# Kernel tuning notes

Measured on AMD Instinct MI355X. Metric: run time of the kernel, lower is better.

The kernel has to match this reference:

```python
import jax, jax.numpy as jnp
import numpy as np


def setup_inputs() -> dict:
    key = jax.random.key(0)
    kq, kk, kv = jax.random.split(key, 3)
    B, H, S, D = 2, 16, 2048, 128
    return {
        "q": jax.random.normal(kq, (B, H, S, D), dtype=jnp.float32),
        "k": jax.random.normal(kk, (B, H, S, D), dtype=jnp.float32),
        "v": jax.random.normal(kv, (B, H, S, D), dtype=jnp.float32),
    }


def reference(q, k, v):
    # scaled dot-product attention with causal mask (dropout in eval mode -> identity)
    d_k = k.shape[-1]
    scale = 1.0 / jnp.sqrt(jnp.asarray(d_k, dtype=q.dtype))
    # [B,H,Sq,Skv]
    attn = jnp.einsum("bhqd,bhkd->bhqk", q, k) * scale
    Sq = q.shape[-2]
    causal = jnp.triu(jnp.ones((Sq, Sq), dtype=bool), k=1)  # True above diagonal -> masked
    attn = jnp.where(causal, -jnp.inf, attn)
    attn = jax.nn.softmax(attn, axis=-1)
    return jnp.einsum("bhqk,bhkd->bhqd", attn, v)
```

## Files before the change

### kernel.cpp

```cpp
#include <hip/hip_runtime.h>

#define SQ 2048
#define DH 128
#define KVB 64
#define BHN 32
#define ELEMS ((size_t)BHN * SQ * DH)

typedef __bf16 bf16x8 __attribute__((ext_vector_type(8)));
typedef float f32x16 __attribute__((ext_vector_type(16)));

__device__ __forceinline__ f32x16 mfma32(bf16x8 a, bf16x8 b, f32x16 c){
  return __builtin_amdgcn_mfma_f32_32x32x16_bf16(a, b, c, 0, 0, 0);
}

#define EXP2 __builtin_amdgcn_exp2f
#define GLD16(g, l) __builtin_amdgcn_global_load_lds( \
    (const __attribute__((address_space(1))) void*)(g), \
    (__attribute__((address_space(3))) void*)(l), 16, 0, 0)
#define VMCNT0 asm volatile("s_waitcnt vmcnt(0)" ::: "memory")
#define VMCNT4 asm volatile("s_waitcnt vmcnt(4)" ::: "memory")
#define VMCNT8 asm volatile("s_waitcnt vmcnt(8)" ::: "memory")
#define BARRIER asm volatile("s_barrier" ::: "memory")

__device__ __forceinline__ unsigned short f2bf(float f){
  unsigned u = __builtin_bit_cast(unsigned, f);
  u += 0x7fffu + ((u >> 16) & 1u);
  return (unsigned short)(u >> 16);
}
__device__ __forceinline__ unsigned packbf(float a, float b){
  return (unsigned)f2bf(a) | ((unsigned)f2bf(b) << 16);
}

__device__ __forceinline__ void swap32(unsigned a, unsigned b, bool h, unsigned &x, unsigned &y){
  unsigned sb = __shfl_xor(b, 32);
  unsigned sa = __shfl_xor(a, 32);
  x = h ? sb : a;
  y = h ? b : sa;
}

__device__ __forceinline__ bf16x8 mkfrag(unsigned w0, unsigned w1, unsigned w2, unsigned w3){
  uint4 t; t.x = w0; t.y = w1; t.z = w2; t.w = w3;
  return __builtin_bit_cast(bf16x8, t);
}

__global__ __launch_bounds__(256, 4)
void convk(const float* __restrict__ K, unsigned short* __restrict__ Kb){
  const size_t g = (size_t)blockIdx.x * 256 + threadIdx.x;
  #pragma unroll
  for (int i = 0; i < 4; ++i){
    size_t e = (g + (size_t)i * 262144) * 8;
    float4 a = *(const float4*)(K + e);
    float4 b = *(const float4*)(K + e + 4);
    uint4 o;
    o.x = packbf(a.x, a.y); o.y = packbf(a.z, a.w);
    o.z = packbf(b.x, b.y); o.w = packbf(b.z, b.w);
    *(uint4*)(Kb + e) = o;
  }
}

__global__ __launch_bounds__(256, 4)
void convvt(const float* __restrict__ V, unsigned short* __restrict__ Vt){
  __shared__ unsigned short T[64][65];
  const int bidx = blockIdx.x;
  const int dt = bidx & 1;
  const int kt = (bidx >> 1) & 31;
  const int bh = bidx >> 6;
  const float* src = V + (size_t)bh*SQ*DH + (size_t)kt*64*DH + dt*64;
  unsigned short* dst = Vt + (size_t)bh*DH*SQ + (size_t)dt*64*SQ + kt*64;
  const int t = threadIdx.x;
  const int c4 = (t & 15) * 4;
  const int r0 = t >> 4;
  #pragma unroll
  for (int i = 0; i < 4; ++i){
    int r = r0 + i*16;
    float4 f = *(const float4*)(src + (size_t)r*DH + c4);
    T[r][c4+0] = f2bf(f.x); T[r][c4+1] = f2bf(f.y);
    T[r][c4+2] = f2bf(f.z); T[r][c4+3] = f2bf(f.w);
  }
  __syncthreads();
  #pragma unroll
  for (int i = 0; i < 4; ++i){
    int d = r0 + i*16;
    ushort4 w;
    w.x = T[c4+0][d]; w.y = T[c4+1][d]; w.z = T[c4+2][d]; w.w = T[c4+3][d];
    *(ushort4*)(dst + (size_t)d*SQ + c4) = w;
  }
}

__global__ __launch_bounds__(512, 2)
void attn_fwd_gl(const float* __restrict__ Q,
                 const unsigned short* __restrict__ Kbg,
                 const unsigned short* __restrict__ Vtg,
                 float* __restrict__ O)
{
  __shared__ __align__(16) unsigned char smem[131072];
  float* SF = (float*)smem;

  const int tid  = threadIdx.x;
  const int lane = tid & 63;
  const int wid  = tid >> 6;
  const int rg   = wid & 3;
  const int par  = wid >> 2;
  const int col  = lane & 31;
  const int hi   = lane >> 5;

  const int b   = blockIdx.x;
  const int xcd = b & 7;
  const int seq = b >> 3;
  const int bh4 = seq & 3;
  const int j   = seq >> 2;
  const int bh  = xcd + 8*bh4;

  const size_t base = (size_t)bh * SQ * DH;
  const float* Qg = Q + base;
  const unsigned short* Kb = Kbg + base;
  const unsigned short* Vt = Vtg + base;
  float* Og = O + base;

  const float SC = 0.08838834764831845f * 1.4426950408889634f;

  const unsigned short* ksrc[2];
  const unsigned short* vsrc[2];
  int kdst[2], vdst[2];
  #pragma unroll
  for (int i = 0; i < 2; ++i){
    int c = i*512 + tid;
    int r = c >> 4, dc = c & 15;
    ksrc[i] = Kb + (size_t)r*DH + ((dc ^ (r & 7)) * 8);
    kdst[i] = c * 16;
    int d = c >> 3, f = c & 7;
    vsrc[i] = Vt + (size_t)d*SQ + ((f ^ ((d >> 1) & 7)) * 8);
    vdst[i] = 16384 + c * 16;
  }

  auto LOADT = [&](int kvb, int bsel){
    const int bboff = bsel * 32768;
    #pragma unroll
    for (int i = 0; i < 2; ++i){
      GLD16(ksrc[i] + (size_t)kvb * DH, &smem[bboff + kdst[i]]);
      GLD16(vsrc[i] + kvb,              &smem[bboff + vdst[i]]);
    }
  };

  #pragma unroll 1
  for (int ph = 0; ph < 2; ++ph){
    const int qt = ph ? j : (15 - j);
    const int nt = 2*qt + 2;
    const int Q0 = qt*128 + rg*32;
    const int qg = Q0 + col;

    bf16x8 qf[8];
    #pragma unroll
    for (int dc = 0; dc < 8; ++dc){
      const float* src = Qg + (size_t)qg*DH + dc*16 + hi*8;
      float4 f0 = *(const float4*)(src);
      float4 f1 = *(const float4*)(src + 4);
      uint4 tq;
      tq.x = packbf(f0.x*SC, f0.y*SC); tq.y = packbf(f0.z*SC, f0.w*SC);
      tq.z = packbf(f1.x*SC, f1.y*SC); tq.w = packbf(f1.z*SC, f1.w*SC);
      qf[dc] = __builtin_bit_cast(bf16x8, tq);
    }

    f32x16 o0 = {}, o1 = {}, o2 = {}, o3 = {};
    float m = -1e30f, lsum = 0.f;

    LOADT(0, 0);
    if (nt > 1) LOADT(KVB, 1);
    if (nt > 2) LOADT(2*KVB, 2);
    if (nt > 2){ VMCNT8; } else { VMCNT4; }
    BARRIER;

    #pragma unroll 1
    for (int t = 0; t < nt; ++t){
      const int kvb = t * KVB;
      const int bboff = (t & 3) * 32768;
      const int myk = kvb + par*32;

      if (t + 3 < nt) LOADT(kvb + 3*KVB, (t + 3) & 3);

      if (myk <= Q0 + 31){
        f32x16 s0 = {};
        const int krow = par*32 + col;
        #pragma unroll
        for (int dc = 0; dc < 8; ++dc){
          uint4 rk = *(const uint4*)&smem[bboff + krow*256 + ((dc*32 + hi*16) ^ ((krow & 7) << 4))];
          s0 = mfma32(__builtin_bit_cast(bf16x8, rk), qf[dc], s0);
        }

        if (myk + 31 > Q0){
          #pragma unroll
          for (int r = 0; r < 16; ++r){
            int kl = (r & 3) + 8*(r >> 2) + 4*hi;
            if (myk + kl > qg) s0[r] = -1e30f;
          }
        }

        float tmax = -1e30f;
        #pragma unroll
        for (int r = 0; r < 16; ++r) tmax = fmaxf(tmax, s0[r]);
        tmax = fmaxf(tmax, __shfl_xor(tmax, 32));
        if (!__all(tmax <= m + 8.0f)){
          float mnew  = fmaxf(m, tmax);
          float alpha = EXP2(m - mnew);
          m = mnew;
          lsum *= alpha;
          o0 *= alpha; o1 *= alpha; o2 *= alpha; o3 *= alpha;
        }

        float ps = 0.f;
        #pragma unroll
        for (int r = 0; r < 16; ++r){ float e = EXP2(s0[r] - m); s0[r] = e; ps += e; }
        lsum += ps;

        unsigned ua0 = packbf(s0[0],  s0[1]),  ua1 = packbf(s0[2],  s0[3]);
        unsigned ua2 = packbf(s0[4],  s0[5]),  ua3 = packbf(s0[6],  s0[7]);
        unsigned ua4 = packbf(s0[8],  s0[9]),  ua5 = packbf(s0[10], s0[11]);
        unsigned ua6 = packbf(s0[12], s0[13]), ua7 = packbf(s0[14], s0[15]);
        bool h = (bool)hi;
        unsigned w0, w1, w2, w3;
        bf16x8 pf[2];
        swap32(ua0, ua2, h, w0, w2); swap32(ua1, ua3, h, w1, w3); pf[0] = mkfrag(w0,w1,w2,w3);
        swap32(ua4, ua6, h, w0, w2); swap32(ua5, ua7, h, w1, w3); pf[1] = mkfrag(w0,w1,w2,w3);

        #pragma unroll
        for (int cc = 0; cc < 2; ++cc){
          #pragma unroll
          for (int db = 0; db < 4; ++db){
            int rowd = db*32 + col;
            uint4 rv = *(const uint4*)&smem[bboff + 16384 + rowd*128 + ((par*64 + cc*32 + hi*16) ^ (((rowd >> 1) & 7) << 4))];
            f32x16& oo = (db==0)?o0:(db==1)?o1:(db==2)?o2:o3;
            oo = mfma32(__builtin_bit_cast(bf16x8, rv), pf[cc], oo);
          }
        }
      }

      if (t + 1 < nt){
        const int rem = nt - 2 - t;
        if (rem >= 2){ VMCNT8; } else if (rem == 1){ VMCNT4; } else { VMCNT0; }
      }
      BARRIER;
    }

    lsum += __shfl_xor(lsum, 32);

    float a0 = 1.f, a1 = 0.f, inv = 0.f;
    #pragma unroll 1
    for (int round = 0; round < 2; ++round){
      const f32x16& pa = round ? o2 : o0;
      const f32x16& pb = round ? o3 : o1;
      if (par == 1){
        #pragma unroll
        for (int i2 = 0; i2 < 16; ++i2){
          SF[rg*2048 + i2*64 + lane]      = pa[i2];
          SF[rg*2048 + (16+i2)*64 + lane] = pb[i2];
        }
        if (round == 0){
          SF[8192 + rg*64 + lane] = m;
          SF[8448 + rg*64 + lane] = lsum;
        }
      }
      __syncthreads();
      if (par == 0){
        if (round == 0){
          float m1 = SF[8192 + rg*64 + lane];
          float l1 = SF[8448 + rg*64 + lane];
          float ms = fmaxf(m, m1);
          a0 = EXP2(m - ms);
          a1 = EXP2(m1 - ms);
          float ls = lsum*a0 + l1*a1;
          inv = 1.0f / ls;
        }
        #pragma unroll
        for (int dbi = 0; dbi < 2; ++dbi){
          const f32x16& oo = round ? (dbi ? o3 : o2) : (dbi ? o1 : o0);
          const int db = round*2 + dbi;
          #pragma unroll
          for (int rg2 = 0; rg2 < 4; ++rg2){
            float4 w;
            w.x = (oo[rg2*4+0]*a0 + SF[rg*2048 + (dbi*16 + rg2*4+0)*64 + lane]*a1) * inv;
            w.y = (oo[rg2*4+1]*a0 + SF[rg*2048 + (dbi*16 + rg2*4+1)*64 + lane]*a1) * inv;
            w.z = (oo[rg2*4+2]*a0 + SF[rg*2048 + (dbi*16 + rg2*4+2)*64 + lane]*a1) * inv;
            w.w = (oo[rg2*4+3]*a0 + SF[rg*2048 + (dbi*16 + rg2*4+3)*64 + lane]*a1) * inv;
            *(float4*)(Og + (size_t)qg*DH + db*32 + rg2*8 + hi*4) = w;
          }
        }
      }
      __syncthreads();
    }
  }
}

__global__ __launch_bounds__(512, 2)
void attn_fwd_fb(const float* __restrict__ Q,
                 const float* __restrict__ Kf,
                 const float* __restrict__ Vf,
                 float* __restrict__ O)
{
  __shared__ __align__(16) unsigned char smem[65536];
  float* SF = (float*)smem;
  const int tid  = threadIdx.x;
  const int lane = tid & 63;
  const int wid  = tid >> 6;
  const int rg   = wid & 3;
  const int par  = wid >> 2;
  const int col  = lane & 31;
  const int hi   = lane >> 5;
  const int i4   = lane & 3;
  const int d0   = (lane >> 2)*8;
  const int b   = blockIdx.x;
  const int xcd = b & 7;
  const int seq = b >> 3;
  const int bh4 = seq & 3;
  const int j   = seq >> 2;
  const int bh  = xcd + 8*bh4;
  const size_t base = (size_t)bh * SQ * DH;
  const float* Qg = Q + base;
  const float* Kg = Kf + base;
  const float* Vg = Vf + base;
  float* Og = O + base;
  const float SC = 0.08838834764831845f * 1.4426950408889634f;
  float4 kr[4], vr[4];
  auto LOADT = [&](int kvb){
    #pragma unroll
    for (int i2 = 0; i2 < 2; ++i2){
      int c = i2*512 + tid, r = c >> 4, dc = c & 15;
      const float* src = Kg + (size_t)(kvb + r)*DH + dc*8;
      kr[2*i2]   = *(const float4*)(src);
      kr[2*i2+1] = *(const float4*)(src + 4);
    }
    #pragma unroll
    for (int it = 0; it < 2; ++it){
      int row = wid*8 + it*4 + i4;
      const float* src = Vg + (size_t)(kvb + row)*DH + d0;
      vr[2*it]   = *(const float4*)(src);
      vr[2*it+1] = *(const float4*)(src + 4);
    }
  };
  auto STORET = [&](int bsel){
    const int bboff = bsel * 32768;
    #pragma unroll
    for (int i2 = 0; i2 < 2; ++i2){
      int c = i2*512 + tid, r = c >> 4, dc = c & 15;
      uint4 kv;
      kv.x = packbf(kr[2*i2].x,   kr[2*i2].y);
      kv.y = packbf(kr[2*i2].z,   kr[2*i2].w);
      kv.z = packbf(kr[2*i2+1].x, kr[2*i2+1].y);
      kv.w = packbf(kr[2*i2+1].z, kr[2*i2+1].w);
      *(uint4*)&smem[bboff + r*256 + ((dc*16) ^ ((r & 7) << 4))] = kv;
    }
    #pragma unroll
    for (int it = 0; it < 2; ++it){
      int r0 = wid*8 + it*4;
      unsigned M0 = packbf(vr[2*it].x,   vr[2*it].y);
      unsigned M1 = packbf(vr[2*it].z,   vr[2*it].w);
      unsigned M2 = packbf(vr[2*it+1].x, vr[2*it+1].y);
      unsigned M3 = packbf(vr[2*it+1].z, vr[2*it+1].w);
      unsigned t0=__shfl_xor(M1,1), t1=__shfl_xor(M0,1), t2=__shfl_xor(M3,1), t3=__shfl_xor(M2,1);
      bool ob1 = i4 & 1;
      unsigned N0 = ob1 ? t0 : M0;
      unsigned N1 = ob1 ? M1 : t1;
      unsigned N2 = ob1 ? t2 : M2;
      unsigned N3 = ob1 ? M3 : t3;
      unsigned u0s=__shfl_xor(N2,2), u1s=__shfl_xor(N3,2), u2s=__shfl_xor(N0,2), u3s=__shfl_xor(N1,2);
      bool ob2 = i4 & 2;
      unsigned F0 = ob2 ? u0s : N0;
      unsigned F1 = ob2 ? u1s : N1;
      unsigned F2 = ob2 ? N2 : u2s;
      unsigned F3 = ob2 ? N3 : u3s;
      int d = d0 + 2*i4;
      unsigned lo0 = (F0 & 0xffffu) | (F1 << 16);
      unsigned lo1 = (F2 & 0xffffu) | (F3 << 16);
      unsigned hi0 = (F0 >> 16) | (F1 & 0xffff0000u);
      unsigned hi1 = (F2 >> 16) | (F3 & 0xffff0000u);
      int cb = r0*2;
      int sA = ((d >> 1) & 7) << 4;
      *(uint2*)&smem[bboff + 16384 + d*128     + (cb ^ sA)] = make_uint2(lo0, lo1);
      *(uint2*)&smem[bboff + 16384 + (d+1)*128 + (cb ^ sA)] = make_uint2(hi0, hi1);
    }
  };
  #pragma unroll 1
  for (int ph = 0; ph < 2; ++ph){
    const int qt = ph ? j : (15 - j);
    const int nt = 2*qt + 2;
    const int Q0 = qt*128 + rg*32;
    const int qg = Q0 + col;
    bf16x8 qf[8];
    #pragma unroll
    for (int dc = 0; dc < 8; ++dc){
      const float* src = Qg + (size_t)qg*DH + dc*16 + hi*8;
      float4 f0 = *(const float4*)(src);
      float4 f1 = *(const float4*)(src + 4);
      uint4 tq;
      tq.x = packbf(f0.x*SC, f0.y*SC); tq.y = packbf(f0.z*SC, f0.w*SC);
      tq.z = packbf(f1.x*SC, f1.y*SC); tq.w = packbf(f1.z*SC, f1.w*SC);
      qf[dc] = __builtin_bit_cast(bf16x8, tq);
    }
    f32x16 o0 = {}, o1 = {}, o2 = {}, o3 = {};
    float m = -1e30f, lsum = 0.f;
    LOADT(0);
    STORET(0);
    __syncthreads();
    #pragma unroll 1
    for (int t = 0; t < nt; ++t){
      const int kvb = t * KVB;
      const int bboff = (t & 1) * 32768;
      const int myk = kvb + par*32;
      if (t + 1 < nt) LOADT(kvb + KVB);
      if (myk <= Q0 + 31){
        f32x16 s0 = {};
        const int krow = par*32 + col;
        #pragma unroll
        for (int dc = 0; dc < 8; ++dc){
          uint4 rk = *(const uint4*)&smem[bboff + krow*256 + ((dc*32 + hi*16) ^ ((krow & 7) << 4))];
          s0 = mfma32(__builtin_bit_cast(bf16x8, rk), qf[dc], s0);
        }
        if (myk + 31 > Q0){
          #pragma unroll
          for (int r = 0; r < 16; ++r){
            int kl = (r & 3) + 8*(r >> 2) + 4*hi;
            if (myk + kl > qg) s0[r] = -1e30f;
          }
        }
        float tmax = -1e30f;
        #pragma unroll
        for (int r = 0; r < 16; ++r) tmax = fmaxf(tmax, s0[r]);
        tmax = fmaxf(tmax, __shfl_xor(tmax, 32));
        if (!__all(tmax <= m + 8.0f)){
          float mnew  = fmaxf(m, tmax);
          float alpha = EXP2(m - mnew);
          m = mnew;
          lsum *= alpha;
          o0 *= alpha; o1 *= alpha; o2 *= alpha; o3 *= alpha;
        }
        float ps = 0.f;
        #pragma unroll
        for (int r = 0; r < 16; ++r){ float e = EXP2(s0[r] - m); s0[r] = e; ps += e; }
        lsum += ps;
        unsigned ua0 = packbf(s0[0],  s0[1]),  ua1 = packbf(s0[2],  s0[3]);
        unsigned ua2 = packbf(s0[4],  s0[5]),  ua3 = packbf(s0[6],  s0[7]);
        unsigned ua4 = packbf(s0[8],  s0[9]),  ua5 = packbf(s0[10], s0[11]);
        unsigned ua6 = packbf(s0[12], s0[13]), ua7 = packbf(s0[14], s0[15]);
        bool h = (bool)hi;
        unsigned w0, w1, w2, w3;
        bf16x8 pf[2];
        swap32(ua0, ua2, h, w0, w2); swap32(ua1, ua3, h, w1, w3); pf[0] = mkfrag(w0,w1,w2,w3);
        swap32(ua4, ua6, h, w0, w2); swap32(ua5, ua7, h, w1, w3); pf[1] = mkfrag(w0,w1,w2,w3);
        #pragma unroll
        for (int cc = 0; cc < 2; ++cc){
          #pragma unroll
          for (int db = 0; db < 4; ++db){
            int rowd = db*32 + col;
            uint4 rv = *(const uint4*)&smem[bboff + 16384 + rowd*128 + ((par*64 + cc*32 + hi*16) ^ (((rowd >> 1) & 7) << 4))];
            f32x16& oo = (db==0)?o0:(db==1)?o1:(db==2)?o2:o3;
            oo = mfma32(__builtin_bit_cast(bf16x8, rv), pf[cc], oo);
          }
        }
      }
      if (t + 1 < nt) STORET((t + 1) & 1);
      __syncthreads();
    }
    lsum += __shfl_xor(lsum, 32);
    float a0 = 1.f, a1 = 0.f, inv = 0.f;
    #pragma unroll 1
    for (int round = 0; round < 2; ++round){
      const f32x16& pa = round ? o2 : o0;
      const f32x16& pb = round ? o3 : o1;
      if (par == 1){
        #pragma unroll
        for (int i2 = 0; i2 < 16; ++i2){
          SF[rg*2048 + i2*64 + lane]      = pa[i2];
          SF[rg*2048 + (16+i2)*64 + lane] = pb[i2];
        }
        if (round == 0){
          SF[8192 + rg*64 + lane] = m;
          SF[8448 + rg*64 + lane] = lsum;
        }
      }
      __syncthreads();
      if (par == 0){
        if (round == 0){
          float m1 = SF[8192 + rg*64 + lane];
          float l1 = SF[8448 + rg*64 + lane];
          float ms = fmaxf(m, m1);
          a0 = EXP2(m - ms);
          a1 = EXP2(m1 - ms);
          float ls = lsum*a0 + l1*a1;
          inv = 1.0f / ls;
        }
        #pragma unroll
        for (int dbi = 0; dbi < 2; ++dbi){
          const f32x16& oo = round ? (dbi ? o3 : o2) : (dbi ? o1 : o0);
          const int db = round*2 + dbi;
          #pragma unroll
          for (int rg2 = 0; rg2 < 4; ++rg2){
            float4 w;
            w.x = (oo[rg2*4+0]*a0 + SF[rg*2048 + (dbi*16 + rg2*4+0)*64 + lane]*a1) * inv;
            w.y = (oo[rg2*4+1]*a0 + SF[rg*2048 + (dbi*16 + rg2*4+1)*64 + lane]*a1) * inv;
            w.z = (oo[rg2*4+2]*a0 + SF[rg*2048 + (dbi*16 + rg2*4+2)*64 + lane]*a1) * inv;
            w.w = (oo[rg2*4+3]*a0 + SF[rg*2048 + (dbi*16 + rg2*4+3)*64 + lane]*a1) * inv;
            *(float4*)(Og + (size_t)qg*DH + db*32 + rg2*8 + hi*4) = w;
          }
        }
      }
      __syncthreads();
    }
  }
}

extern "C" void kernel_launch(void* const* d_in, const int* in_sizes, int n_in,
                              void* d_out, int out_size, void* d_ws, size_t ws_size,
                              hipStream_t stream) {
  const float* q = (const float*)d_in[0];
  const float* k = (const float*)d_in[1];
  const float* v = (const float*)d_in[2];
  float* out = (float*)d_out;

  const size_t need = 2 * ELEMS * sizeof(unsigned short);
  if (ws_size >= need){
    unsigned short* kb = (unsigned short*)d_ws;
    unsigned short* vt = kb + ELEMS;
    convk<<<1024, 256, 0, stream>>>(k, kb);
    convvt<<<2048, 256, 0, stream>>>(v, vt);
    attn_fwd_gl<<<256, 512, 0, stream>>>(q, kb, vt, out);
  } else {
    attn_fwd_fb<<<256, 512, 0, stream>>>(q, k, v, out);
  }
}
```

Before: 92.00 us.

## Software-pipeline PV of previous tile with QK of current tile

Restructures the attention loop so that each iteration issues the P·V MFMAs for the previous KV tile alongside the Q·K MFMAs for the current tile. The goal is to hide the softmax and exp latency behind matrix work, with s_setprio raising wave priority around the MFMA block. The P fragments and the previous buffer offset now live across iterations, and a final P·V drain runs after the loop. Prefetch depth drops from three tiles ahead to two, with waitcnts adjusted, which trades some load-latency hiding for a ring slot kept live for the delayed P·V read.

```diff
diff --git a/kernel.cpp b/kernel.cpp
--- a/kernel.cpp
+++ b/kernel.cpp
@@ -19,7 +19,6 @@
     (__attribute__((address_space(3))) void*)(l), 16, 0, 0)
 #define VMCNT0 asm volatile("s_waitcnt vmcnt(0)" ::: "memory")
 #define VMCNT4 asm volatile("s_waitcnt vmcnt(4)" ::: "memory")
-#define VMCNT8 asm volatile("s_waitcnt vmcnt(8)" ::: "memory")
 #define BARRIER asm volatile("s_barrier" ::: "memory")
 
 __device__ __forceinline__ unsigned short f2bf(float f){
@@ -163,11 +162,13 @@
 
     f32x16 o0 = {}, o1 = {}, o2 = {}, o3 = {};
     float m = -1e30f, lsum = 0.f;
+    bf16x8 pf0 = {}, pf1 = {};
+    bool pvalid = false;
+    int  prevbb = 0;
 
     LOADT(0, 0);
-    if (nt > 1) LOADT(KVB, 1);
-    if (nt > 2) LOADT(2*KVB, 2);
-    if (nt > 2){ VMCNT8; } else { VMCNT4; }
+    LOADT(KVB, 1);
+    VMCNT4;
     BARRIER;
 
     #pragma unroll 1
@@ -175,18 +176,36 @@
       const int kvb = t * KVB;
       const int bboff = (t & 3) * 32768;
       const int myk = kvb + par*32;
-
-      if (t + 3 < nt) LOADT(kvb + 3*KVB, (t + 3) & 3);
-
-      if (myk <= Q0 + 31){
-        f32x16 s0 = {};
+      const bool qvalid = (myk <= Q0 + 31);
+
+      if (t + 2 < nt) LOADT(kvb + 2*KVB, (t + 2) & 3);
+
+      f32x16 s0 = {};
+      __builtin_amdgcn_s_setprio(1);
+      if (pvalid){
+        #pragma unroll
+        for (int cc = 0; cc < 2; ++cc){
+          bf16x8 pf = cc ? pf1 : pf0;
+          #pragma unroll
+          for (int db = 0; db < 4; ++db){
+            int rowd = db*32 + col;
+            uint4 rv = *(const uint4*)&smem[prevbb + 16384 + rowd*128 + ((par*64 + cc*32 + hi*16) ^ (((rowd >> 1) & 7) << 4))];
+            f32x16& oo = (db==0)?o0:(db==1)?o1:(db==2)?o2:o3;
+            oo = mfma32(__builtin_bit_cast(bf16x8, rv), pf, oo);
+          }
+        }
+      }
+      if (qvalid){
         const int krow = par*32 + col;
         #pragma unroll
         for (int dc = 0; dc < 8; ++dc){
           uint4 rk = *(const uint4*)&smem[bboff + krow*256 + ((dc*32 + hi*16) ^ ((krow & 7) << 4))];
           s0 = mfma32(__builtin_bit_cast(bf16x8, rk), qf[dc], s0);
         }
-
+      }
+      __builtin_amdgcn_s_setprio(0);
+
+      if (qvalid){
         if (myk + 31 > Q0){
           #pragma unroll
           for (int r = 0; r < 16; ++r){
@@ -218,28 +237,34 @@
         unsigned ua6 = packbf(s0[12], s0[13]), ua7 = packbf(s0[14], s0[15]);
         bool h = (bool)hi;
         unsigned w0, w1, w2, w3;
-        bf16x8 pf[2];
-        swap32(ua0, ua2, h, w0, w2); swap32(ua1, ua3, h, w1, w3); pf[0] = mkfrag(w0,w1,w2,w3);
-        swap32(ua4, ua6, h, w0, w2); swap32(ua5, ua7, h, w1, w3); pf[1] = mkfrag(w0,w1,w2,w3);
-
-        #pragma unroll
-        for (int cc = 0; cc < 2; ++cc){
-          #pragma unroll
-          for (int db = 0; db < 4; ++db){
-            int rowd = db*32 + col;
-            uint4 rv = *(const uint4*)&smem[bboff + 16384 + rowd*128 + ((par*64 + cc*32 + hi*16) ^ (((rowd >> 1) & 7) << 4))];
-            f32x16& oo = (db==0)?o0:(db==1)?o1:(db==2)?o2:o3;
-            oo = mfma32(__builtin_bit_cast(bf16x8, rv), pf[cc], oo);
-          }
-        }
-      }
+        swap32(ua0, ua2, h, w0, w2); swap32(ua1, ua3, h, w1, w3); pf0 = mkfrag(w0,w1,w2,w3);
+        swap32(ua4, ua6, h, w0, w2); swap32(ua5, ua7, h, w1, w3); pf1 = mkfrag(w0,w1,w2,w3);
+      }
+      pvalid = qvalid;
+      prevbb = bboff;
 
       if (t + 1 < nt){
-        const int rem = nt - 2 - t;
-        if (rem >= 2){ VMCNT8; } else if (rem == 1){ VMCNT4; } else { VMCNT0; }
+        if (t + 2 < nt){ VMCNT4; } else { VMCNT0; }
       }
       BARRIER;
     }
+
+    __builtin_amdgcn_s_setprio(1);
+    if (pvalid){
+      #pragma unroll
+      for (int cc = 0; cc < 2; ++cc){
+        bf16x8 pf = cc ? pf1 : pf0;
+        #pragma unroll
+        for (int db = 0; db < 4; ++db){
+          int rowd = db*32 + col;
+          uint4 rv = *(const uint4*)&smem[prevbb + 16384 + rowd*128 + ((par*64 + cc*32 + hi*16) ^ (((rowd >> 1) & 7) << 4))];
+          f32x16& oo = (db==0)?o0:(db==1)?o1:(db==2)?o2:o3;
+          oo = mfma32(__builtin_bit_cast(bf16x8, rv), pf, oo);
+        }
+      }
+    }
+    __builtin_amdgcn_s_setprio(0);
+    __syncthreads();
 
     lsum += __shfl_xor(lsum, 32);
 
```

New measurement: 94.00 us. 1.02x slower.

## Merge K/V conversion launches and use permlane32 swap for cross-half exchanges

Applied to the files above, without the earlier changes.

Combines the K bf16 conversion and V transpose-conversion kernels into one launch with a block-index split, removing a kernel launch and its tail gap. In the attention inner loop, the ds_bpermute-based __shfl_xor(…,32) exchanges for the row max, P fragment repacking and final lsum are replaced by the v_permlane32_swap instruction. The max reduction is also rewritten as a tree to shorten the dependency chain. The permlane swap semantics must match the old select-based swap; they do if the instruction swaps the upper half of the first operand with the lower half of the second.

```diff
diff --git a/kernel.cpp b/kernel.cpp
--- a/kernel.cpp
+++ b/kernel.cpp
@@ -8,6 +8,7 @@
 
 typedef __bf16 bf16x8 __attribute__((ext_vector_type(8)));
 typedef float f32x16 __attribute__((ext_vector_type(16)));
+typedef unsigned uint2v __attribute__((ext_vector_type(2)));
 
 __device__ __forceinline__ f32x16 mfma32(bf16x8 a, bf16x8 b, f32x16 c){
   return __builtin_amdgcn_mfma_f32_32x32x16_bf16(a, b, c, 0, 0, 0);
@@ -31,6 +32,29 @@
   return (unsigned)f2bf(a) | ((unsigned)f2bf(b) << 16);
 }
 
+#if __has_builtin(__builtin_amdgcn_permlane32_swap)
+__device__ __forceinline__ void swap32p(unsigned a, unsigned b, unsigned &x, unsigned &y){
+  uint2v r = __builtin_amdgcn_permlane32_swap(a, b, false, false);
+  x = r[0]; y = r[1];
+}
+#else
+__device__ __forceinline__ void swap32p(unsigned a, unsigned b, unsigned &x, unsigned &y){
+  x = a; y = b;
+  asm volatile("" : "+v"(x), "+v"(y));
+  asm("v_permlane32_swap_b32 %0, %1" : "+v"(x), "+v"(y));
+}
+#endif
+__device__ __forceinline__ float halfmax(float t){
+  unsigned u = __builtin_bit_cast(unsigned, t), x, y;
+  swap32p(u, u, x, y);
+  return fmaxf(__builtin_bit_cast(float, x), __builtin_bit_cast(float, y));
+}
+__device__ __forceinline__ float halfadd(float t){
+  unsigned u = __builtin_bit_cast(unsigned, t), x, y;
+  swap32p(u, u, x, y);
+  return __builtin_bit_cast(float, x) + __builtin_bit_cast(float, y);
+}
+
 __device__ __forceinline__ void swap32(unsigned a, unsigned b, bool h, unsigned &x, unsigned &y){
   unsigned sb = __shfl_xor(b, 32);
   unsigned sa = __shfl_xor(a, 32);
@@ -44,46 +68,46 @@
 }
 
 __global__ __launch_bounds__(256, 4)
-void convk(const float* __restrict__ K, unsigned short* __restrict__ Kb){
-  const size_t g = (size_t)blockIdx.x * 256 + threadIdx.x;
-  #pragma unroll
-  for (int i = 0; i < 4; ++i){
-    size_t e = (g + (size_t)i * 262144) * 8;
-    float4 a = *(const float4*)(K + e);
-    float4 b = *(const float4*)(K + e + 4);
-    uint4 o;
-    o.x = packbf(a.x, a.y); o.y = packbf(a.z, a.w);
-    o.z = packbf(b.x, b.y); o.w = packbf(b.z, b.w);
-    *(uint4*)(Kb + e) = o;
-  }
-}
-
-__global__ __launch_bounds__(256, 4)
-void convvt(const float* __restrict__ V, unsigned short* __restrict__ Vt){
-  __shared__ unsigned short T[64][65];
-  const int bidx = blockIdx.x;
-  const int dt = bidx & 1;
-  const int kt = (bidx >> 1) & 31;
-  const int bh = bidx >> 6;
-  const float* src = V + (size_t)bh*SQ*DH + (size_t)kt*64*DH + dt*64;
-  unsigned short* dst = Vt + (size_t)bh*DH*SQ + (size_t)dt*64*SQ + kt*64;
-  const int t = threadIdx.x;
-  const int c4 = (t & 15) * 4;
-  const int r0 = t >> 4;
-  #pragma unroll
-  for (int i = 0; i < 4; ++i){
-    int r = r0 + i*16;
-    float4 f = *(const float4*)(src + (size_t)r*DH + c4);
-    T[r][c4+0] = f2bf(f.x); T[r][c4+1] = f2bf(f.y);
-    T[r][c4+2] = f2bf(f.z); T[r][c4+3] = f2bf(f.w);
-  }
-  __syncthreads();
-  #pragma unroll
-  for (int i = 0; i < 4; ++i){
-    int d = r0 + i*16;
-    ushort4 w;
-    w.x = T[c4+0][d]; w.y = T[c4+1][d]; w.z = T[c4+2][d]; w.w = T[c4+3][d];
-    *(ushort4*)(dst + (size_t)d*SQ + c4) = w;
+void convkvt(const float* __restrict__ K, const float* __restrict__ V,
+             unsigned short* __restrict__ Kb, unsigned short* __restrict__ Vt){
+  if (blockIdx.x < 1024){
+    const size_t g = (size_t)blockIdx.x * 256 + threadIdx.x;
+    #pragma unroll
+    for (int i = 0; i < 4; ++i){
+      size_t e = (g + (size_t)i * 262144) * 8;
+      float4 a = *(const float4*)(K + e);
+      float4 b = *(const float4*)(K + e + 4);
+      uint4 o;
+      o.x = packbf(a.x, a.y); o.y = packbf(a.z, a.w);
+      o.z = packbf(b.x, b.y); o.w = packbf(b.z, b.w);
+      *(uint4*)(Kb + e) = o;
+    }
+  } else {
+    __shared__ unsigned short T[64][65];
+    const int bidx = blockIdx.x - 1024;
+    const int dt = bidx & 1;
+    const int kt = (bidx >> 1) & 31;
+    const int bh = bidx >> 6;
+    const float* src = V + (size_t)bh*SQ*DH + (size_t)kt*64*DH + dt*64;
+    unsigned short* dst = Vt + (size_t)bh*DH*SQ + (size_t)dt*64*SQ + kt*64;
+    const int t = threadIdx.x;
+    const int c4 = (t & 15) * 4;
+    const int r0 = t >> 4;
+    #pragma unroll
+    for (int i = 0; i < 4; ++i){
+      int r = r0 + i*16;
+      float4 f = *(const float4*)(src + (size_t)r*DH + c4);
+      T[r][c4+0] = f2bf(f.x); T[r][c4+1] = f2bf(f.y);
+      T[r][c4+2] = f2bf(f.z); T[r][c4+3] = f2bf(f.w);
+    }
+    __syncthreads();
+    #pragma unroll
+    for (int i = 0; i < 4; ++i){
+      int d = r0 + i*16;
+      ushort4 w;
+      w.x = T[c4+0][d]; w.y = T[c4+1][d]; w.z = T[c4+2][d]; w.w = T[c4+3][d];
+      *(ushort4*)(dst + (size_t)d*SQ + c4) = w;
+    }
   }
 }
 
@@ -195,10 +219,13 @@
           }
         }
 
-        float tmax = -1e30f;
-        #pragma unroll
-        for (int r = 0; r < 16; ++r) tmax = fmaxf(tmax, s0[r]);
-        tmax = fmaxf(tmax, __shfl_xor(tmax, 32));
+        float p0 = fmaxf(s0[0],  s0[1]),  p1 = fmaxf(s0[2],  s0[3]);
+        float p2 = fmaxf(s0[4],  s0[5]),  p3 = fmaxf(s0[6],  s0[7]);
+        float p4 = fmaxf(s0[8],  s0[9]),  p5 = fmaxf(s0[10], s0[11]);
+        float p6 = fmaxf(s0[12], s0[13]), p7 = fmaxf(s0[14], s0[15]);
+        float q0v = fmaxf(p0, p1), q1v = fmaxf(p2, p3);
+        float q2v = fmaxf(p4, p5), q3v = fmaxf(p6, p7);
+        float tmax = halfmax(fmaxf(fmaxf(q0v, q1v), fmaxf(q2v, q3v)));
         if (!__all(tmax <= m + 8.0f)){
           float mnew  = fmaxf(m, tmax);
           float alpha = EXP2(m - mnew);
@@ -216,11 +243,10 @@
         unsigned ua2 = packbf(s0[4],  s0[5]),  ua3 = packbf(s0[6],  s0[7]);
         unsigned ua4 = packbf(s0[8],  s0[9]),  ua5 = packbf(s0[10], s0[11]);
         unsigned ua6 = packbf(s0[12], s0[13]), ua7 = packbf(s0[14], s0[15]);
-        bool h = (bool)hi;
         unsigned w0, w1, w2, w3;
         bf16x8 pf[2];
-        swap32(ua0, ua2, h, w0, w2); swap32(ua1, ua3, h, w1, w3); pf[0] = mkfrag(w0,w1,w2,w3);
-        swap32(ua4, ua6, h, w0, w2); swap32(ua5, ua7, h, w1, w3); pf[1] = mkfrag(w0,w1,w2,w3);
+        swap32p(ua0, ua2, w0, w2); swap32p(ua1, ua3, w1, w3); pf[0] = mkfrag(w0,w1,w2,w3);
+        swap32p(ua4, ua6, w0, w2); swap32p(ua5, ua7, w1, w3); pf[1] = mkfrag(w0,w1,w2,w3);
 
         #pragma unroll
         for (int cc = 0; cc < 2; ++cc){
@@ -241,7 +267,7 @@
       BARRIER;
     }
 
-    lsum += __shfl_xor(lsum, 32);
+    lsum = halfadd(lsum);
 
     float a0 = 1.f, a1 = 0.f, inv = 0.f;
     #pragma unroll 1
@@ -519,8 +545,7 @@
   if (ws_size >= need){
     unsigned short* kb = (unsigned short*)d_ws;
     unsigned short* vt = kb + ELEMS;
-    convk<<<1024, 256, 0, stream>>>(k, kb);
-    convvt<<<2048, 256, 0, stream>>>(v, vt);
+    convkvt<<<3072, 256, 0, stream>>>(k, v, kb, vt);
     attn_fwd_gl<<<256, 512, 0, stream>>>(q, kb, vt, out);
   } else {
     attn_fwd_fb<<<256, 512, 0, stream>>>(q, k, v, out);
```

Result: faster. 89.09 us (-3.2%).
